# Optimization experiments

Hardware: AMD Instinct MI355X
Metric: run time of the kernel (lower is better)

Reference implementation:

```python
import jax, jax.numpy as jnp
import numpy as np

N, D, E, R, TOPK = 8192, 4096, 8, 128, 2
LORA_ALPHA = 32.0
SCALING = LORA_ALPHA / R


def setup_inputs() -> dict:
    key = jax.random.key(0)
    kx, kr, ka, kb = jax.random.split(key, 4)
    x = jax.random.normal(kx, (N, D), jnp.float32)
    Wr = jax.random.normal(kr, (E, D), jnp.float32) * 0.02  # router Linear weight [E, D]
    br = jnp.zeros((E,), jnp.float32)                        # router bias
    A = jax.random.normal(ka, (E, R, D), jnp.float32) * 0.02  # per-expert lora_A weights
    B = jax.random.normal(kb, (E, D, R), jnp.float32) * 0.02  # per-expert lora_B weights
    return {"x": x, "Wr": Wr, "br": br, "A": A, "B": B}


def reference(x, Wr, br, A, B):
    # Router: softmax over expert logits, top-k, renormalize selected probs.
    logits = x @ Wr.T + br                       # [N, E]
    probs = jax.nn.softmax(logits, axis=-1)
    top_v, top_i = jax.lax.top_k(probs, TOPK)    # [N, K]
    w = top_v / jnp.sum(top_v, axis=-1, keepdims=True)
    # Scatter renormalized weights back to a dense [N, E] gate (0 for unselected).
    n_idx = jnp.arange(x.shape[0])[:, None]
    gate = jnp.zeros_like(probs).at[n_idx, top_i].set(w)
    # Expert LoRA: y_e = (x @ A_e^T) @ B_e^T * scaling; combine with gates.
    h = jnp.einsum('nd,erd->ner', x, A)          # [N, E, R] small rank intermediate
    out = jnp.einsum('ner,ne,eor->no', h, gate, B) * SCALING  # [N, D]
    return out
```

## Files before the change

### kernel.cpp

```cpp
#include <hip/hip_runtime.h>

#define N_TOK 8192
#define DIM   4096
#define NEXP  8
#define RANK  128
#define EK    (NEXP * RANK)
#define SCAL  0.25f

typedef unsigned short u16;
typedef __bf16 bf16x8 __attribute__((ext_vector_type(8)));
typedef float  f32x4  __attribute__((ext_vector_type(4)));

typedef const __attribute__((address_space(1))) void* as1_cvp;
typedef __attribute__((address_space(3))) void*       as3_vp;

__device__ __forceinline__ void async16(void* lds, const void* g) {
  __builtin_amdgcn_global_load_lds((as1_cvp)g, (as3_vp)lds, 16, 0, 0);
}

__device__ __forceinline__ u16 f2bf(float f) {
  unsigned int u = __builtin_bit_cast(unsigned int, f);
  u += 0x7fffu + ((u >> 16) & 1u);
  return (u16)(u >> 16);
}

__device__ __forceinline__ f32x4 mfma16(bf16x8 a, bf16x8 b, f32x4 c) {
  return __builtin_amdgcn_mfma_f32_16x16x32_bf16(a, b, c, 0, 0, 0);
}

__global__ __launch_bounds__(256) void cvtA_kernel(const float* __restrict__ A,
                                                   u16* __restrict__ Ab) {
  size_t i = (size_t)blockIdx.x * 256 + threadIdx.x;
  float4 v = ((const float4*)A)[i];
  ushort4 o;
  o.x = f2bf(v.x); o.y = f2bf(v.y); o.z = f2bf(v.z); o.w = f2bf(v.w);
  ((ushort4*)Ab)[i] = o;
}

__global__ __launch_bounds__(256) void cvtB_kernel(const float* __restrict__ B,
                                                   u16* __restrict__ Bt) {
  size_t i = (size_t)blockIdx.x * 256 + threadIdx.x;
  int r4 = (int)(i & 31);
  int o_ = (int)((i >> 5) & 4095);
  int e  = (int)(i >> 17);
  float4 v = ((const float4*)B)[i];
  ushort4 u;
  u.x = f2bf(v.x); u.y = f2bf(v.y); u.z = f2bf(v.z); u.w = f2bf(v.w);
  ((ushort4*)Bt)[(size_t)o_ * 256 + e * 32 + r4] = u;
}

__device__ __forceinline__ void router_finalize(
    int n, const float* l_in, const float* __restrict__ br,
    float* __restrict__ gw, int* __restrict__ sel) {
  float l[NEXP];
#pragma unroll
  for (int e = 0; e < NEXP; ++e) l[e] = l_in[e] + br[e];
  int i0 = 0;
#pragma unroll
  for (int e = 1; e < NEXP; ++e) if (l[e] > l[i0]) i0 = e;
  int i1 = (i0 == 0) ? 1 : 0;
#pragma unroll
  for (int e = 0; e < NEXP; ++e) if (e != i0 && l[e] > l[i1]) i1 = e;
  float w0 = 1.f / (1.f + expf(l[i1] - l[i0]));
  gw[n * 2 + 0] = w0 * SCAL;
  gw[n * 2 + 1] = (1.f - w0) * SCAL;
  sel[n] = i0 | (i1 << 4);
}

__global__ __launch_bounds__(256) void router_kernel(
    const float* __restrict__ x, const float* __restrict__ Wr,
    const float* __restrict__ br, u16* __restrict__ xb,
    float* __restrict__ gw, int* __restrict__ sel) {
  const int tid = threadIdx.x;
  const int wv = tid >> 6, lane = tid & 63;
  const int n0 = (blockIdx.x * 4 + wv) * 2;
  const float4* x4 = (const float4*)x;
  const float4* w4 = (const float4*)Wr;

  const float4* xr0 = x4 + (size_t)n0 * 1024;
  const float4* xr1 = x4 + (size_t)(n0 + 1) * 1024;
  ushort4* xo0 = (ushort4*)(xb + (size_t)n0 * DIM);
  ushort4* xo1 = (ushort4*)(xb + (size_t)(n0 + 1) * DIM);

  float s0[NEXP] = {}, s1[NEXP] = {};
#pragma unroll 4
  for (int it = 0; it < 16; ++it) {
    const int col = it * 64 + lane;
    float4 xv0 = xr0[col];
    float4 xv1 = xr1[col];
    ushort4 o0, o1;
    o0.x = f2bf(xv0.x); o0.y = f2bf(xv0.y); o0.z = f2bf(xv0.z); o0.w = f2bf(xv0.w);
    o1.x = f2bf(xv1.x); o1.y = f2bf(xv1.y); o1.z = f2bf(xv1.z); o1.w = f2bf(xv1.w);
    xo0[col] = o0;
    xo1[col] = o1;
#pragma unroll
    for (int e = 0; e < NEXP; ++e) {
      float4 wv4 = w4[(size_t)e * 1024 + col];
      s0[e] += xv0.x * wv4.x + xv0.y * wv4.y + xv0.z * wv4.z + xv0.w * wv4.w;
      s1[e] += xv1.x * wv4.x + xv1.y * wv4.y + xv1.z * wv4.z + xv1.w * wv4.w;
    }
  }
#pragma unroll
  for (int m = 1; m < 64; m <<= 1)
#pragma unroll
    for (int e = 0; e < NEXP; ++e) {
      s0[e] += __shfl_xor(s0[e], m, 64);
      s1[e] += __shfl_xor(s1[e], m, 64);
    }
  if (lane == 0)      router_finalize(n0,     s0, br, gw, sel);
  else if (lane == 1) router_finalize(n0 + 1, s1, br, gw, sel);
}

__global__ __launch_bounds__(512) void listbuild_kernel(
    const int* __restrict__ sel, int* __restrict__ lists,
    int* __restrict__ cnt) {
  __shared__ int blkCnt[NEXP];
  __shared__ int gBase[NEXP];
  __shared__ int waveOff[8][NEXP];
  const int tid = threadIdx.x;
  const int wv = tid >> 6, lane = tid & 63;
  const int n = blockIdx.x * 512 + tid;
  if (tid < NEXP) blkCnt[tid] = 0;
  __syncthreads();
  const int s = sel[n];
  const int i0 = s & 15, i1 = (s >> 4) & 15;
#pragma unroll
  for (int e = 0; e < NEXP; ++e) {
    unsigned long long m0 = __ballot(i0 == e);
    unsigned long long m1 = __ballot(i1 == e);
    if (lane == 0)
      waveOff[wv][e] = atomicAdd(&blkCnt[e], __popcll(m0) + __popcll(m1));
  }
  __syncthreads();
  if (tid < NEXP) gBase[tid] = atomicAdd(&cnt[tid], blkCnt[tid]);
  __syncthreads();
  const unsigned long long lt = (1ull << lane) - 1;
#pragma unroll
  for (int e = 0; e < NEXP; ++e) {
    unsigned long long m0 = __ballot(i0 == e);
    unsigned long long m1 = __ballot(i1 == e);
    int base = gBase[e] + waveOff[wv][e];
    if (i0 == e) lists[e * N_TOK + base + (int)__popcll(m0 & lt)] = n * 2;
    if (i1 == e)
      lists[e * N_TOK + base + (int)__popcll(m0) + (int)__popcll(m1 & lt)] =
          n * 2 + 1;
  }
}

__global__ __launch_bounds__(256) void gemm1_kernel(
    const u16* __restrict__ xb, const u16* __restrict__ Ab,
    const int* __restrict__ lists, const int* __restrict__ cnt,
    const float* __restrict__ gw, u16* __restrict__ G) {
  const int e = blockIdx.y;
  const int mt = blockIdx.x;
  const int c = cnt[e];
  if (mt * 64 >= c) return;

  __shared__ alignas(16) u16 As[64 * 64];
  __shared__ alignas(16) u16 Bs[128 * 64];
  __shared__ int   tokS[64];
  __shared__ float wS[64];

  const int tid = threadIdx.x;
  if (tid < 64) {
    int idx = mt * 64 + tid;
    int ci = idx < c ? idx : (c - 1);
    int entry = lists[e * N_TOK + ci];
    tokS[tid] = entry >> 1;
    wS[tid] = (idx < c) ? gw[entry] : 0.0f;
  }
  __syncthreads();

  const int lr = tid >> 3;
  const int cg = tid & 7;
  const u16* ga0 = xb + (size_t)tokS[lr] * DIM + cg * 8;
  const u16* ga1 = xb + (size_t)tokS[lr + 32] * DIM + cg * 8;
  const u16* gb  = Ab + (size_t)e * (RANK * DIM) + (size_t)lr * DIM + cg * 8;

  const int lane = tid & 63, wvi = tid >> 6;
  const int wm = wvi >> 1, wn = wvi & 1;
  const int m16 = lane & 15, quad = lane >> 4;

  f32x4 acc[2][4] = {};

  for (int k0 = 0; k0 < DIM; k0 += 64) {
    async16(&As[tid * 8], ga0 + k0);
    async16(&As[tid * 8 + 2048], ga1 + k0);
#pragma unroll
    for (int r = 0; r < 4; ++r)
      async16(&Bs[tid * 8 + r * 2048], gb + (size_t)r * 32 * DIM + k0);
    __syncthreads();
#pragma unroll
    for (int ks = 0; ks < 2; ++ks) {
      const int ko = ks * 32 + quad * 8;
      bf16x8 af[2], bfr[4];
#pragma unroll
      for (int i = 0; i < 2; ++i)
        af[i] = *(const bf16x8*)&As[(wm * 32 + i * 16 + m16) * 64 + ko];
#pragma unroll
      for (int j = 0; j < 4; ++j)
        bfr[j] = *(const bf16x8*)&Bs[(wn * 64 + j * 16 + m16) * 64 + ko];
#pragma unroll
      for (int i = 0; i < 2; ++i)
#pragma unroll
        for (int j = 0; j < 4; ++j) acc[i][j] = mfma16(af[i], bfr[j], acc[i][j]);
    }
    __syncthreads();
  }

#pragma unroll
  for (int i = 0; i < 2; ++i)
#pragma unroll
    for (int rr = 0; rr < 4; ++rr) {
      int row = wm * 32 + i * 16 + quad * 4 + rr;
      if (mt * 64 + row < c) {
        int tk = tokS[row];
        float wgt = wS[row];
        u16* gp = G + (size_t)tk * EK + e * RANK + wn * 64 + m16;
#pragma unroll
        for (int j = 0; j < 4; ++j) gp[j * 16] = f2bf(acc[i][j][rr] * wgt);
      }
    }
}

__global__ __launch_bounds__(256) void gemm2_kernel(
    const u16* __restrict__ G, const u16* __restrict__ Bt,
    float* __restrict__ out) {
  const int bx = blockIdx.x;
  const int by = blockIdx.y;
  __shared__ alignas(16) u16 As[128 * 64];
  __shared__ alignas(16) u16 Bs[128 * 64];

  const int tid = threadIdx.x;
  const int lr = tid >> 3, cg = tid & 7;
  const u16* ga = G  + (size_t)(by * 128 + lr) * EK + cg * 8;
  const u16* gb = Bt + (size_t)(bx * 128 + lr) * EK + cg * 8;

  const int lane = tid & 63, wvi = tid >> 6;
  const int wm = wvi >> 1, wn = wvi & 1;
  const int m16 = lane & 15, quad = lane >> 4;

  f32x4 acc[4][4] = {};

  for (int k0 = 0; k0 < EK; k0 += 64) {
#pragma unroll
    for (int r = 0; r < 4; ++r) {
      async16(&As[tid * 8 + r * 2048], ga + (size_t)r * 32 * EK + k0);
      async16(&Bs[tid * 8 + r * 2048], gb + (size_t)r * 32 * EK + k0);
    }
    __syncthreads();
#pragma unroll
    for (int ks = 0; ks < 2; ++ks) {
      const int ko = ks * 32 + quad * 8;
      bf16x8 af[4], bfr[4];
#pragma unroll
      for (int i = 0; i < 4; ++i)
        af[i] = *(const bf16x8*)&As[(wm * 64 + i * 16 + m16) * 64 + ko];
#pragma unroll
      for (int j = 0; j < 4; ++j)
        bfr[j] = *(const bf16x8*)&Bs[(wn * 64 + j * 16 + m16) * 64 + ko];
#pragma unroll
      for (int i = 0; i < 4; ++i)
#pragma unroll
        for (int j = 0; j < 4; ++j) acc[i][j] = mfma16(af[i], bfr[j], acc[i][j]);
    }
    __syncthreads();
  }

#pragma unroll
  for (int i = 0; i < 4; ++i)
#pragma unroll
    for (int rr = 0; rr < 4; ++rr) {
      int row = by * 128 + wm * 64 + i * 16 + quad * 4 + rr;
      float* op = out + (size_t)row * DIM + bx * 128 + wn * 64 + m16;
#pragma unroll
      for (int j = 0; j < 4; ++j) op[j * 16] = acc[i][j][rr];
    }
}

extern "C" void kernel_launch(void* const* d_in, const int* in_sizes, int n_in,
                              void* d_out, int out_size, void* d_ws, size_t ws_size,
                              hipStream_t stream) {
  const float* x  = (const float*)d_in[0];
  const float* Wr = (const float*)d_in[1];
  const float* br = (const float*)d_in[2];
  const float* A  = (const float*)d_in[3];
  const float* B  = (const float*)d_in[4];
  float* out = (float*)d_out;

  char* w = (char*)d_ws;
  u16* xb = (u16*)w;      w += (size_t)N_TOK * DIM * 2;
  u16* G  = (u16*)w;      w += (size_t)N_TOK * EK * 2;
  u16* Ab = (u16*)w;      w += (size_t)NEXP * RANK * DIM * 2;
  u16* Bt = (u16*)w;      w += (size_t)DIM * EK * 2;
  float* gw = (float*)w;  w += (size_t)N_TOK * 2 * 4;
  int* lists = (int*)w;   w += (size_t)NEXP * N_TOK * 4;
  int* sel = (int*)w;     w += (size_t)N_TOK * 4;
  int* cnt = (int*)w;     w += 256;

  hipMemsetAsync(cnt, 0, NEXP * sizeof(int), stream);
  hipMemsetAsync(G, 0, (size_t)N_TOK * EK * 2, stream);

  cvtA_kernel<<<dim3(4096), dim3(256), 0, stream>>>(A, Ab);
  cvtB_kernel<<<dim3(4096), dim3(256), 0, stream>>>(B, Bt);
  router_kernel<<<dim3(1024), dim3(256), 0, stream>>>(x, Wr, br, xb, gw, sel);
  listbuild_kernel<<<dim3(16), dim3(512), 0, stream>>>(sel, lists, cnt);
  gemm1_kernel<<<dim3(128, NEXP), dim3(256), 0, stream>>>(xb, Ab, lists, cnt, gw, G);
  gemm2_kernel<<<dim3(32, 64), dim3(256), 0, stream>>>(G, Bt, out);
}
```

Measured before the change: 501.2 us.

## Rewrite gemm2 with 256x256 tiles, 4-stage async LDS ring and block swizzle

The second GEMM (dense gate-weighted rank activations times transposed B) now uses 512-thread blocks computing 256x256 output tiles. A 4-slot ring of async global-to-LDS loads with K=32 steps keeps three stages in flight, waiting through explicit vmcnt and s_barrier instead of a full sync around each single-buffered step. Block indices are swizzled to group tiles for L2 reuse, and MFMA sections get raised wave priority. This aims to hide load latency and cut redundant G/Bt traffic, at the cost of more accumulator registers per thread and more LDS per block.

```diff
diff --git a/kernel.cpp b/kernel.cpp
--- a/kernel.cpp
+++ b/kernel.cpp
@@ -27,6 +27,17 @@
 __device__ __forceinline__ f32x4 mfma16(bf16x8 a, bf16x8 b, f32x4 c) {
   return __builtin_amdgcn_mfma_f32_16x16x32_bf16(a, b, c, 0, 0, 0);
 }
+
+#define PIPE_WAIT(N)                                            \
+  __builtin_amdgcn_sched_barrier(0);                            \
+  asm volatile("s_waitcnt vmcnt(" #N ")" ::: "memory");         \
+  __builtin_amdgcn_s_barrier();                                 \
+  __builtin_amdgcn_sched_barrier(0)
+
+#define PIPE_END()                                              \
+  __builtin_amdgcn_sched_barrier(0);                            \
+  __builtin_amdgcn_s_barrier();                                 \
+  __builtin_amdgcn_sched_barrier(0)
 
 __global__ __launch_bounds__(256) void cvtA_kernel(const float* __restrict__ A,
                                                    u16* __restrict__ Ab) {
@@ -223,56 +234,76 @@
     }
 }
 
-__global__ __launch_bounds__(256) void gemm2_kernel(
+__global__ __launch_bounds__(512, 2) void gemm2_kernel(
     const u16* __restrict__ G, const u16* __restrict__ Bt,
     float* __restrict__ out) {
-  const int bx = blockIdx.x;
-  const int by = blockIdx.y;
-  __shared__ alignas(16) u16 As[128 * 64];
-  __shared__ alignas(16) u16 Bs[128 * 64];
+  __shared__ alignas(16) u16 ring[4][2][256 * 32];
+
+  const int lin = blockIdx.y * 16 + blockIdx.x;
+  const int swz = (lin & 7) * 64 + (lin >> 3);
+  const int by = swz >> 4;
+  const int bx = swz & 15;
 
   const int tid = threadIdx.x;
-  const int lr = tid >> 3, cg = tid & 7;
-  const u16* ga = G  + (size_t)(by * 128 + lr) * EK + cg * 8;
-  const u16* gb = Bt + (size_t)(bx * 128 + lr) * EK + cg * 8;
+  const int sr = tid >> 2;
+  const int sc = (tid & 3) * 8;
+  const u16* gA = G  + (size_t)(by * 256 + sr) * EK + sc;
+  const u16* gB = Bt + (size_t)(bx * 256 + sr) * EK + sc;
 
   const int lane = tid & 63, wvi = tid >> 6;
-  const int wm = wvi >> 1, wn = wvi & 1;
+  const int wm = wvi >> 2, wn = wvi & 3;
   const int m16 = lane & 15, quad = lane >> 4;
 
-  f32x4 acc[4][4] = {};
-
-  for (int k0 = 0; k0 < EK; k0 += 64) {
-#pragma unroll
-    for (int r = 0; r < 4; ++r) {
-      async16(&As[tid * 8 + r * 2048], ga + (size_t)r * 32 * EK + k0);
-      async16(&Bs[tid * 8 + r * 2048], gb + (size_t)r * 32 * EK + k0);
-    }
-    __syncthreads();
-#pragma unroll
-    for (int ks = 0; ks < 2; ++ks) {
-      const int ko = ks * 32 + quad * 8;
-      bf16x8 af[4], bfr[4];
-#pragma unroll
-      for (int i = 0; i < 4; ++i)
-        af[i] = *(const bf16x8*)&As[(wm * 64 + i * 16 + m16) * 64 + ko];
-#pragma unroll
-      for (int j = 0; j < 4; ++j)
-        bfr[j] = *(const bf16x8*)&Bs[(wn * 64 + j * 16 + m16) * 64 + ko];
-#pragma unroll
-      for (int i = 0; i < 4; ++i)
-#pragma unroll
-        for (int j = 0; j < 4; ++j) acc[i][j] = mfma16(af[i], bfr[j], acc[i][j]);
-    }
-    __syncthreads();
-  }
-
-#pragma unroll
-  for (int i = 0; i < 4; ++i)
+  f32x4 acc[8][4] = {};
+
+  auto STAGE = [&](int kt, int slot) {
+    u16* lA = &ring[slot][0][tid * 8];
+    u16* lB = &ring[slot][1][tid * 8];
+    const u16* sA = gA + kt * 32;
+    const u16* sB = gB + kt * 32;
+    async16(lA,        sA);
+    async16(lA + 4096, sA + (size_t)128 * EK);
+    async16(lB,        sB);
+    async16(lB + 4096, sB + (size_t)128 * EK);
+  };
+
+  auto COMPUTE = [&](int slot) {
+    const u16* As_ = &ring[slot][0][0];
+    const u16* Bs_ = &ring[slot][1][0];
+    bf16x8 bfr[4];
+#pragma unroll
+    for (int j = 0; j < 4; ++j)
+      bfr[j] = *(const bf16x8*)&Bs_[(wn * 64 + j * 16 + m16) * 32 + quad * 8];
+    __builtin_amdgcn_s_setprio(1);
+#pragma unroll
+    for (int i = 0; i < 8; ++i) {
+      bf16x8 af = *(const bf16x8*)&As_[(wm * 128 + i * 16 + m16) * 32 + quad * 8];
+#pragma unroll
+      for (int j = 0; j < 4; ++j) acc[i][j] = mfma16(af, bfr[j], acc[i][j]);
+    }
+    __builtin_amdgcn_s_setprio(0);
+  };
+
+  STAGE(0, 0);
+  STAGE(1, 1);
+  STAGE(2, 2);
+
+  for (int t = 0; t < 29; ++t) {
+    PIPE_WAIT(8);
+    STAGE(t + 3, (t + 3) & 3);
+    COMPUTE(t & 3);
+    PIPE_END();
+  }
+  PIPE_WAIT(8); COMPUTE(1); PIPE_END();
+  PIPE_WAIT(4); COMPUTE(2); PIPE_END();
+  PIPE_WAIT(0); COMPUTE(3); PIPE_END();
+
+#pragma unroll
+  for (int i = 0; i < 8; ++i)
 #pragma unroll
     for (int rr = 0; rr < 4; ++rr) {
-      int row = by * 128 + wm * 64 + i * 16 + quad * 4 + rr;
-      float* op = out + (size_t)row * DIM + bx * 128 + wn * 64 + m16;
+      int row = by * 256 + wm * 128 + i * 16 + quad * 4 + rr;
+      float* op = out + (size_t)row * DIM + bx * 256 + wn * 64 + m16;
 #pragma unroll
       for (int j = 0; j < 4; ++j) op[j * 16] = acc[i][j][rr];
     }
@@ -306,5 +337,5 @@
   router_kernel<<<dim3(1024), dim3(256), 0, stream>>>(x, Wr, br, xb, gw, sel);
   listbuild_kernel<<<dim3(16), dim3(512), 0, stream>>>(sel, lists, cnt);
   gemm1_kernel<<<dim3(128, NEXP), dim3(256), 0, stream>>>(xb, Ab, lists, cnt, gw, G);
-  gemm2_kernel<<<dim3(32, 64), dim3(256), 0, stream>>>(G, Bt, out);
-}
+  gemm2_kernel<<<dim3(16, 32), dim3(512), 0, stream>>>(G, Bt, out);
+}
```

After: 475.2 us. 5.2% less time.
